# Kernel tuning notes

Measured on AMD Instinct MI355X. Metric: run time of the kernel, lower is better.

The kernel has to match this reference:

```python
import jax, jax.numpy as jnp
import numpy as np

N_NODES = 100000
N_EDGES = 1600000
D_IN = 128
D_OUT = 64
NUM_LAYERS = 3
BN_EPS = 1e-5


def setup_inputs() -> dict:
    key = jax.random.key(0)
    k_x, k_e, k_w = jax.random.split(key, 3)
    x = jax.random.normal(k_x, (N_NODES, D_IN), dtype=jnp.float32)
    edge_index = jax.random.randint(k_e, (2, N_EDGES), 0, N_NODES, dtype=jnp.int64)
    bn_gamma = jnp.ones((NUM_LAYERS, D_IN), dtype=jnp.float32)
    bn_beta = jnp.zeros((NUM_LAYERS, D_IN), dtype=jnp.float32)
    W = jax.random.normal(k_w, (D_IN, D_OUT), dtype=jnp.float32) * (1.0 / np.sqrt(D_IN))
    b = jnp.zeros((D_OUT,), dtype=jnp.float32)
    return {"x": x, "edge_index": edge_index, "bn_gamma": bn_gamma, "bn_beta": bn_beta, "W": W, "b": b}


def reference(x, edge_index, bn_gamma, bn_beta, W, b):
    # GNN forward, task='node', aggregate='sum', combine='sum', readout='sum',
    # recursive_weighting=False, training mode (no sigmoid, BN uses batch stats).
    n = x.shape[0]
    dst = edge_index[0]  # spmm(Adj, h): pooled[i] = sum over edges (i <- j) of h[j]
    src = edge_index[1]
    h = x
    for layer in range(NUM_LAYERS):
        # neighbor aggregate: sparse spmm == gather + segment-sum scatter
        agg = jax.ops.segment_sum(h[src], dst, num_segments=n)  # [N, D]
        # graph readout (single batched graph): sum over nodes, broadcast to every node
        readout = jnp.sum(h, axis=0, keepdims=True)  # [1, D]
        # functional 'sum' combine of (self, aggregated, readout)
        h = h + agg + readout
        # BatchNorm1d over the node dimension (training statistics, biased var)
        mean = jnp.mean(h, axis=0)
        var = jnp.var(h, axis=0)
        h = (h - mean) * jax.lax.rsqrt(var + BN_EPS) * bn_gamma[layer] + bn_beta[layer]
        h = jax.nn.relu(h)
    # node-task head (training branch: raw logits)
    return h @ W + b
```

## Files before the change

kernel.cpp:

```cpp
#include <hip/hip_runtime.h>

#define D 128
#define DOUT 64
#define BN_EPS 1e-5f
#define BCAP 96

#define NBK_SHIFT 8
#define NBK_MAX   512
#define SLOT_CAP  704
#define PA_E      4000

typedef unsigned int   u32;
typedef unsigned short u16;
typedef short  short8 __attribute__((ext_vector_type(8)));
typedef float  f32x4  __attribute__((ext_vector_type(4)));

__device__ __forceinline__ u16 f2bf(float f) {
    u32 x = __float_as_uint(f);
    x += 0x7fffu + ((x >> 16) & 1u);
    return (u16)(x >> 16);
}
__device__ __forceinline__ float bflo(u32 u) { return __uint_as_float(u << 16); }
__device__ __forceinline__ float bfhi(u32 u) { return __uint_as_float(u & 0xffff0000u); }

__global__ void init_kernel(const float* __restrict__ x, u16* __restrict__ xb,
                            int* __restrict__ bcnt,
                            float* __restrict__ sums,
                            const float* __restrict__ W, u16* __restrict__ wt,
                            int n_nodes, int n_ctr) {
    int total = n_nodes * (D / 4);
    for (int t = blockIdx.x * blockDim.x + threadIdx.x; t < total;
         t += gridDim.x * blockDim.x) {
        float4 v = ((const float4*)x)[t];
        ((ushort4*)xb)[t] = make_ushort4(f2bf(v.x), f2bf(v.y), f2bf(v.z), f2bf(v.w));
        if (t < n_ctr) bcnt[t] = 0;
        if (t < 3 * 8 * 256) sums[t] = 0.f;
        if (t < D * DOUT) {
            int c = t >> 7, k = t & (D - 1);
            wt[t] = f2bf(W[k * DOUT + c]);
        }
    }
}

__global__ __launch_bounds__(256) void partA_kernel(const int* __restrict__ ei,
                             int* __restrict__ bcnt,
                             u32* __restrict__ pairs, int n_edges, int n_bkt) {
    __shared__ u32 ord[PA_E];
    __shared__ u16 obkt[PA_E];
    __shared__ int hist[NBK_MAX];
    __shared__ int scanA[NBK_MAX], scanB[NBK_MAX];
    __shared__ int st[NBK_MAX], cur[NBK_MAX], gbase[NBK_MAX];

    const int tid  = threadIdx.x;
    const int slot = blockIdx.x & 7;
    const int e0   = blockIdx.x * PA_E;
    const int e1   = min(e0 + PA_E, n_edges);

    for (int i = tid; i < NBK_MAX; i += 256) hist[i] = 0;
    __syncthreads();
    for (int e = e0 + tid; e < e1; e += 256)
        atomicAdd(&hist[ei[e] >> NBK_SHIFT], 1);
    __syncthreads();
    for (int i = tid; i < NBK_MAX; i += 256) scanA[i] = hist[i];
    __syncthreads();
    int* a = scanA; int* b = scanB;
    for (int s = 1; s < NBK_MAX; s <<= 1) {
        for (int i = tid; i < NBK_MAX; i += 256)
            b[i] = a[i] + (i >= s ? a[i - s] : 0);
        __syncthreads();
        int* t_ = a; a = b; b = t_;
    }
    for (int x = tid; x < n_bkt; x += 256) {
        int c   = hist[x];
        int stx = a[x] - c;
        st[x] = stx; cur[x] = stx;
        gbase[x] = c ? atomicAdd(&bcnt[((x << 3) + slot) << 4], c) : 0;
    }
    __syncthreads();
    for (int e = e0 + tid; e < e1; e += 256) {
        int d = ei[e];
        int s = ei[n_edges + e];
        int x = d >> NBK_SHIFT;
        int pos = atomicAdd(&cur[x], 1);
        ord[pos]  = ((u32)(d & 255) << 17) | (u32)s;
        obkt[pos] = (u16)x;
    }
    __syncthreads();
    const int cntE = e1 - e0;
    for (int i = tid; i < cntE; i += 256) {
        int x   = obkt[i];
        int pos = gbase[x] + (i - st[x]);
        if (pos < SLOT_CAP)
            pairs[(size_t)((x << 3) + slot) * SLOT_CAP + pos] = ord[i];
    }
}

__global__ __launch_bounds__(256) void partB_kernel(const u32* __restrict__ pairs,
                             const int* __restrict__ bcnt,
                             int* __restrict__ deg, int* __restrict__ srcs,
                             int n_nodes) {
    __shared__ u32 lp[8 * SLOT_CAP];
    __shared__ int lsrc[8 * SLOT_CAP];
    __shared__ int cnt[256], st[256], cur[256];
    __shared__ int scanA[256], scanB[256];
    __shared__ int sofs[9];
    const int tid = threadIdx.x;
    int b = blockIdx.x;
    int node0 = b << NBK_SHIFT;
    if (tid == 0) {
        int acc = 0;
        for (int x = 0; x < 8; ++x) {
            sofs[x] = acc;
            acc += min(bcnt[((b << 3) + x) << 4], SLOT_CAP);
        }
        sofs[8] = acc;
    }
    cnt[tid] = 0;
    __syncthreads();
    for (int x = 0; x < 8; ++x) {
        int c0 = sofs[x], c1 = sofs[x + 1];
        const u32* src = pairs + (size_t)((b << 3) + x) * SLOT_CAP;
        for (int t = tid; t < c1 - c0; t += blockDim.x) {
            u32 pr = src[t];
            lp[c0 + t] = pr;
            atomicAdd(&cnt[pr >> 17], 1);
        }
    }
    __syncthreads();
    scanA[tid] = cnt[tid];
    __syncthreads();
    int* a = scanA; int* bb = scanB;
    for (int s = 1; s < 256; s <<= 1) {
        bb[tid] = a[tid] + (tid >= s ? a[tid - s] : 0);
        __syncthreads();
        int* t_ = a; a = bb; bb = t_;
    }
    st[tid] = a[tid] - cnt[tid];
    cur[tid] = st[tid];
    __syncthreads();
    int cntE = sofs[8];
    for (int t = tid; t < cntE; t += blockDim.x) {
        u32 pr = lp[t];
        int pos = atomicAdd(&cur[pr >> 17], 1);
        lsrc[pos] = (int)(pr & 0x1FFFFu);
    }
    __syncthreads();
    int grp = tid >> 4, lane = tid & 15;
    for (int li = grp; li < 256; li += 16) {
        int node = node0 + li;
        if (node < n_nodes) {
            int dg = cnt[li], s0 = st[li];
            for (int t = lane; t < dg; t += 16) {
                int key = lsrc[s0 + t];
                int rank = 0;
                for (int u = 0; u < dg; ++u) {
                    int o = lsrc[s0 + u];
                    rank += (o < key) || (o == key && u < t);
                }
                if (rank < BCAP) srcs[(size_t)node * BCAP + rank] = key;
            }
            if (lane == 0) deg[node] = dg;
        }
    }
}

template <bool APPLY>
__global__ void agg_kernel(const u16* __restrict__ h,
                           const int* __restrict__ srcs,
                           const int* __restrict__ deg,
                           const float* __restrict__ sums_prev,
                           const float* __restrict__ gam,
                           const float* __restrict__ bet,
                           float* __restrict__ sums_out,
                           u16* __restrict__ vout,
                           int n_nodes, float inv_n) {
    const int lane = threadIdx.x & 15;
    const int grp  = threadIdx.x >> 4;
    const int c    = lane << 3;
    float sc[8], sh[8];
    if (APPLY) {
        #pragma unroll
        for (int k = 0; k < 8; ++k) {
            int f = c + k;
            float S = 0.f, Q = 0.f;
            #pragma unroll
            for (int cp = 0; cp < 8; ++cp) {
                S += sums_prev[cp * 256 + f];
                Q += sums_prev[cp * 256 + 128 + f];
            }
            float mean = S * inv_n;
            float var  = fmaxf(Q * inv_n - mean * mean, 0.f);
            sc[k] = gam[f] * rsqrtf(var + BN_EPS);
            sh[k] = bet[f] - mean * sc[k];
        }
    }
    const int stride = gridDim.x * 16;
    float a[8];
    float s1[8] = {0,0,0,0,0,0,0,0};
    float s2[8] = {0,0,0,0,0,0,0,0};

#define ACC(u_) do { \
    float f0 = bflo((u_).x), f1 = bfhi((u_).x); \
    float f2 = bflo((u_).y), f3 = bfhi((u_).y); \
    float f4 = bflo((u_).z), f5 = bfhi((u_).z); \
    float f6 = bflo((u_).w), f7 = bfhi((u_).w); \
    if (APPLY) { \
        a[0] += fmaxf(fmaf(f0, sc[0], sh[0]), 0.f); \
        a[1] += fmaxf(fmaf(f1, sc[1], sh[1]), 0.f); \
        a[2] += fmaxf(fmaf(f2, sc[2], sh[2]), 0.f); \
        a[3] += fmaxf(fmaf(f3, sc[3], sh[3]), 0.f); \
        a[4] += fmaxf(fmaf(f4, sc[4], sh[4]), 0.f); \
        a[5] += fmaxf(fmaf(f5, sc[5], sh[5]), 0.f); \
        a[6] += fmaxf(fmaf(f6, sc[6], sh[6]), 0.f); \
        a[7] += fmaxf(fmaf(f7, sc[7], sh[7]), 0.f); \
    } else { \
        a[0] += f0; a[1] += f1; a[2] += f2; a[3] += f3; \
        a[4] += f4; a[5] += f5; a[6] += f6; a[7] += f7; \
    } } while (0)

    for (int i = blockIdx.x * 16 + grp; i < n_nodes; i += stride) {
        int off = i * BCAP;
        int dg  = min(deg[i], BCAP);
        {
            uint4 u = *(const uint4*)(h + ((size_t)i << 7) + c);
            float f0 = bflo(u.x), f1 = bfhi(u.x), f2 = bflo(u.y), f3 = bfhi(u.y);
            float f4 = bflo(u.z), f5 = bfhi(u.z), f6 = bflo(u.w), f7 = bfhi(u.w);
            float ff[8] = {f0, f1, f2, f3, f4, f5, f6, f7};
            #pragma unroll
            for (int k = 0; k < 8; ++k)
                a[k] = APPLY ? fmaxf(fmaf(ff[k], sc[k], sh[k]), 0.f) : ff[k];
        }
        for (int base = 0; base < dg; base += 16) {
            int cnt = min(dg - base, 16);
            int sv = (lane < cnt) ? srcs[off + base + lane] : 0;
            int svn = 0;
            int nb = base + 16;
            if (nb < dg && lane < min(dg - nb, 16)) svn = srcs[off + nb + lane];
            int k = 0;
            for (; k + 8 <= cnt; k += 8) {
                int j0 = __shfl(sv, k + 0, 16), j1 = __shfl(sv, k + 1, 16);
                int j2 = __shfl(sv, k + 2, 16), j3 = __shfl(sv, k + 3, 16);
                int j4 = __shfl(sv, k + 4, 16), j5 = __shfl(sv, k + 5, 16);
                int j6 = __shfl(sv, k + 6, 16), j7 = __shfl(sv, k + 7, 16);
                uint4 b0 = *(const uint4*)(h + ((size_t)j0 << 7) + c);
                uint4 b1 = *(const uint4*)(h + ((size_t)j1 << 7) + c);
                uint4 b2 = *(const uint4*)(h + ((size_t)j2 << 7) + c);
                uint4 b3 = *(const uint4*)(h + ((size_t)j3 << 7) + c);
                uint4 b4 = *(const uint4*)(h + ((size_t)j4 << 7) + c);
                uint4 b5 = *(const uint4*)(h + ((size_t)j5 << 7) + c);
                uint4 b6 = *(const uint4*)(h + ((size_t)j6 << 7) + c);
                uint4 b7 = *(const uint4*)(h + ((size_t)j7 << 7) + c);
                ACC(b0); ACC(b1); ACC(b2); ACC(b3);
                ACC(b4); ACC(b5); ACC(b6); ACC(b7);
            }
            for (; k + 4 <= cnt; k += 4) {
                int j0 = __shfl(sv, k + 0, 16), j1 = __shfl(sv, k + 1, 16);
                int j2 = __shfl(sv, k + 2, 16), j3 = __shfl(sv, k + 3, 16);
                uint4 b0 = *(const uint4*)(h + ((size_t)j0 << 7) + c);
                uint4 b1 = *(const uint4*)(h + ((size_t)j1 << 7) + c);
                uint4 b2 = *(const uint4*)(h + ((size_t)j2 << 7) + c);
                uint4 b3 = *(const uint4*)(h + ((size_t)j3 << 7) + c);
                ACC(b0); ACC(b1); ACC(b2); ACC(b3);
            }
            for (; k < cnt; ++k) {
                int j0 = __shfl(sv, k, 16);
                uint4 b0 = *(const uint4*)(h + ((size_t)j0 << 7) + c);
                ACC(b0);
            }
            sv = svn;
        }
        uint4 w;
        w.x = (u32)f2bf(a[0]) | ((u32)f2bf(a[1]) << 16);
        w.y = (u32)f2bf(a[2]) | ((u32)f2bf(a[3]) << 16);
        w.z = (u32)f2bf(a[4]) | ((u32)f2bf(a[5]) << 16);
        w.w = (u32)f2bf(a[6]) | ((u32)f2bf(a[7]) << 16);
        *(uint4*)(vout + ((size_t)i << 7) + c) = w;
        #pragma unroll
        for (int k = 0; k < 8; ++k) {
            s1[k] += a[k];
            s2[k] = fmaf(a[k], a[k], s2[k]);
        }
    }
#undef ACC

    __shared__ float redS[16][128];
    __shared__ float redQ[16][128];
    #pragma unroll
    for (int k = 0; k < 8; ++k) {
        redS[grp][c + k] = s1[k];
        redQ[grp][c + k] = s2[k];
    }
    __syncthreads();
    int tid = threadIdx.x;
    if (tid < 128) {
        float S = 0.f, Q = 0.f;
        #pragma unroll
        for (int g = 0; g < 16; ++g) { S += redS[g][tid]; Q += redQ[g][tid]; }
        int cp = blockIdx.x & 7;
        unsafeAtomicAdd(&sums_out[cp * 256 + tid], S);
        unsafeAtomicAdd(&sums_out[cp * 256 + 128 + tid], Q);
    }
}

__global__ __launch_bounds__(256) void head_mfma_kernel(
        const u16* __restrict__ v2, const float* __restrict__ sums2,
        const float* __restrict__ gam, const float* __restrict__ bet,
        const u16* __restrict__ wt, const float* __restrict__ b,
        float* __restrict__ out, int n_nodes, float inv_n) {
    const int wave = threadIdx.x >> 6;
    const int lane = threadIdx.x & 63;
    const int lo   = lane & 15;
    const int hi   = lane >> 4;

    short8 Bf[4][4];
    #pragma unroll
    for (int ct = 0; ct < 4; ++ct)
        #pragma unroll
        for (int ks = 0; ks < 4; ++ks)
            Bf[ct][ks] = *(const short8*)(wt + (ct * 16 + lo) * D + ks * 32 + hi * 8);

    float sc[4][8], sh[4][8];
    #pragma unroll
    for (int ks = 0; ks < 4; ++ks)
        #pragma unroll
        for (int j = 0; j < 8; ++j) {
            int f = ks * 32 + hi * 8 + j;
            float S = 0.f, Q = 0.f;
            #pragma unroll
            for (int cp = 0; cp < 8; ++cp) {
                S += sums2[cp * 256 + f];
                Q += sums2[cp * 256 + 128 + f];
            }
            float mean = S * inv_n;
            float var  = fmaxf(Q * inv_n - mean * mean, 0.f);
            sc[ks][j] = gam[f] * rsqrtf(var + BN_EPS);
            sh[ks][j] = bet[f] - mean * sc[ks][j];
        }
    float bias[4];
    #pragma unroll
    for (int ct = 0; ct < 4; ++ct) bias[ct] = b[ct * 16 + lo];

    const int nrt = (n_nodes + 15) >> 4;
    for (int rt = blockIdx.x * 4 + wave; rt < nrt; rt += gridDim.x * 4) {
        const int r0 = rt << 4;
        const int ar = min(r0 + lo, n_nodes - 1);
        const u16* hrow = v2 + ((size_t)ar << 7);
        f32x4 acc[4];
        #pragma unroll
        for (int ct = 0; ct < 4; ++ct) acc[ct] = (f32x4){0.f, 0.f, 0.f, 0.f};
        #pragma unroll
        for (int ks = 0; ks < 4; ++ks) {
            uint4 u = *(const uint4*)(hrow + ks * 32 + hi * 8);
            float f0 = bflo(u.x), f1 = bfhi(u.x), f2 = bflo(u.y), f3 = bfhi(u.y);
            float f4 = bflo(u.z), f5 = bfhi(u.z), f6 = bflo(u.w), f7 = bfhi(u.w);
            float w0 = fmaxf(fmaf(f0, sc[ks][0], sh[ks][0]), 0.f);
            float w1 = fmaxf(fmaf(f1, sc[ks][1], sh[ks][1]), 0.f);
            float w2 = fmaxf(fmaf(f2, sc[ks][2], sh[ks][2]), 0.f);
            float w3 = fmaxf(fmaf(f3, sc[ks][3], sh[ks][3]), 0.f);
            float w4 = fmaxf(fmaf(f4, sc[ks][4], sh[ks][4]), 0.f);
            float w5 = fmaxf(fmaf(f5, sc[ks][5], sh[ks][5]), 0.f);
            float w6 = fmaxf(fmaf(f6, sc[ks][6], sh[ks][6]), 0.f);
            float w7 = fmaxf(fmaf(f7, sc[ks][7], sh[ks][7]), 0.f);
            union { uint4 u4; short8 s8; } af;
            af.u4.x = (u32)f2bf(w0) | ((u32)f2bf(w1) << 16);
            af.u4.y = (u32)f2bf(w2) | ((u32)f2bf(w3) << 16);
            af.u4.z = (u32)f2bf(w4) | ((u32)f2bf(w5) << 16);
            af.u4.w = (u32)f2bf(w6) | ((u32)f2bf(w7) << 16);
            #pragma unroll
            for (int ct = 0; ct < 4; ++ct)
                acc[ct] = __builtin_amdgcn_mfma_f32_16x16x32_bf16(
                    af.s8, Bf[ct][ks], acc[ct], 0, 0, 0);
        }
        #pragma unroll
        for (int ct = 0; ct < 4; ++ct)
            #pragma unroll
            for (int rg = 0; rg < 4; ++rg) {
                int r = r0 + hi * 4 + rg;
                if (r < n_nodes)
                    out[(size_t)r * DOUT + ct * 16 + lo] = acc[ct][rg] + bias[ct];
            }
    }
}

extern "C" void kernel_launch(void* const* d_in, const int* in_sizes, int n_in,
                              void* d_out, int out_size, void* d_ws, size_t ws_size,
                              hipStream_t stream) {
    const float* x     = (const float*)d_in[0];
    const int*   ei    = (const int*)d_in[1];
    const float* gamma = (const float*)d_in[2];
    const float* beta  = (const float*)d_in[3];
    const float* W     = (const float*)d_in[4];
    const float* bvec  = (const float*)d_in[5];
    float* out = (float*)d_out;

    const int n_nodes = in_sizes[0] / D;
    const int n_edges = in_sizes[1] / 2;
    const int n_bkt   = (n_nodes + 255) >> 8;
    const int n_ctr   = n_bkt * 8 * 16;

    const size_t row_bytes = (size_t)n_nodes * D * sizeof(u16);
    char* p = (char*)d_ws;
    u16*   xb     = (u16*)p;   p += row_bytes;
    u16*   vA     = (u16*)p;   p += row_bytes;
    u16*   vB     = (u16*)p;   p += row_bytes;
    int*   srcs   = (int*)p;   p += (size_t)n_nodes * BCAP * sizeof(int);
    int*   deg    = (int*)p;   p += (size_t)n_nodes * sizeof(int);
    int*   bcnt   = (int*)p;   p += (size_t)n_ctr * sizeof(int);
    float* sums   = (float*)p;
    u16*   Wt     = (u16*)(p + 3 * 8 * 256 * sizeof(float));
    u32* pairs  = (u32*)vB;

    const float inv_n = 1.0f / (float)n_nodes;

    init_kernel<<<2048, 256, 0, stream>>>(x, xb, bcnt, sums, W, Wt, n_nodes, n_ctr);
    int pa_grid = ((n_edges + PA_E - 1) / PA_E + 7) & ~7;
    partA_kernel<<<pa_grid, 256, 0, stream>>>(ei, bcnt, pairs, n_edges, n_bkt);
    partB_kernel<<<n_bkt, 256, 0, stream>>>(pairs, bcnt, deg, srcs, n_nodes);

    const u16* h = xb;
    u16* vout = vA;
    for (int L = 0; L < 3; ++L) {
        float* sout = sums + (size_t)L * 2048;
        const float* sprev = (L > 0) ? sums + (size_t)(L - 1) * 2048 : nullptr;
        if (L == 0)
            agg_kernel<false><<<4096, 256, 0, stream>>>(h, srcs, deg,
                nullptr, nullptr, nullptr, sout, vout, n_nodes, inv_n);
        else
            agg_kernel<true><<<4096, 256, 0, stream>>>(h, srcs, deg,
                sprev, gamma + (size_t)(L - 1) * D, beta + (size_t)(L - 1) * D,
                sout, vout, n_nodes, inv_n);
        h = vout;
        vout = (vout == vA) ? vB : vA;
    }

    head_mfma_kernel<<<782, 256, 0, stream>>>(h, sums + 2 * 2048,
                                              gamma + 2 * D, beta + 2 * D,
                                              Wt, bvec, out, n_nodes, inv_n);
}
```

Measured before the change: 515.5 us.

## Split BatchNorm statistics out of aggregation kernel and drop 8-way gather unroll

The per-feature sum and sum-of-squares reduction, with its shared-memory buffers and atomics, moves out of agg_kernel into a separate stats_kernel that re-reads the bf16 output after each layer. The 8-wide gather unroll and the prefetch of the next index chunk are removed. The aim is to cut register and LDS pressure in the gather kernel so more waves can hide memory latency. In exchange it adds an extra read of the whole activation buffer plus one more launch per layer. The statistics are now computed from bf16-rounded values rather than fp32 accumulators.

Measured after the change: 460.7 us. -10.6%, faster.

```diff
diff --git a/kernel.cpp b/kernel.cpp
--- a/kernel.cpp
+++ b/kernel.cpp
@@ -171,7 +171,6 @@
                            const float* __restrict__ sums_prev,
                            const float* __restrict__ gam,
                            const float* __restrict__ bet,
-                           float* __restrict__ sums_out,
                            u16* __restrict__ vout,
                            int n_nodes, float inv_n) {
     const int lane = threadIdx.x & 15;
@@ -196,8 +195,6 @@
     }
     const int stride = gridDim.x * 16;
     float a[8];
-    float s1[8] = {0,0,0,0,0,0,0,0};
-    float s2[8] = {0,0,0,0,0,0,0,0};
 
 #define ACC(u_) do { \
     float f0 = bflo((u_).x), f1 = bfhi((u_).x); \
@@ -233,26 +230,7 @@
         for (int base = 0; base < dg; base += 16) {
             int cnt = min(dg - base, 16);
             int sv = (lane < cnt) ? srcs[off + base + lane] : 0;
-            int svn = 0;
-            int nb = base + 16;
-            if (nb < dg && lane < min(dg - nb, 16)) svn = srcs[off + nb + lane];
             int k = 0;
-            for (; k + 8 <= cnt; k += 8) {
-                int j0 = __shfl(sv, k + 0, 16), j1 = __shfl(sv, k + 1, 16);
-                int j2 = __shfl(sv, k + 2, 16), j3 = __shfl(sv, k + 3, 16);
-                int j4 = __shfl(sv, k + 4, 16), j5 = __shfl(sv, k + 5, 16);
-                int j6 = __shfl(sv, k + 6, 16), j7 = __shfl(sv, k + 7, 16);
-                uint4 b0 = *(const uint4*)(h + ((size_t)j0 << 7) + c);
-                uint4 b1 = *(const uint4*)(h + ((size_t)j1 << 7) + c);
-                uint4 b2 = *(const uint4*)(h + ((size_t)j2 << 7) + c);
-                uint4 b3 = *(const uint4*)(h + ((size_t)j3 << 7) + c);
-                uint4 b4 = *(const uint4*)(h + ((size_t)j4 << 7) + c);
-                uint4 b5 = *(const uint4*)(h + ((size_t)j5 << 7) + c);
-                uint4 b6 = *(const uint4*)(h + ((size_t)j6 << 7) + c);
-                uint4 b7 = *(const uint4*)(h + ((size_t)j7 << 7) + c);
-                ACC(b0); ACC(b1); ACC(b2); ACC(b3);
-                ACC(b4); ACC(b5); ACC(b6); ACC(b7);
-            }
             for (; k + 4 <= cnt; k += 4) {
                 int j0 = __shfl(sv, k + 0, 16), j1 = __shfl(sv, k + 1, 16);
                 int j2 = __shfl(sv, k + 2, 16), j3 = __shfl(sv, k + 3, 16);
@@ -267,7 +245,6 @@
                 uint4 b0 = *(const uint4*)(h + ((size_t)j0 << 7) + c);
                 ACC(b0);
             }
-            sv = svn;
         }
         uint4 w;
         w.x = (u32)f2bf(a[0]) | ((u32)f2bf(a[1]) << 16);
@@ -275,30 +252,38 @@
         w.z = (u32)f2bf(a[4]) | ((u32)f2bf(a[5]) << 16);
         w.w = (u32)f2bf(a[6]) | ((u32)f2bf(a[7]) << 16);
         *(uint4*)(vout + ((size_t)i << 7) + c) = w;
-        #pragma unroll
-        for (int k = 0; k < 8; ++k) {
-            s1[k] += a[k];
-            s2[k] = fmaf(a[k], a[k], s2[k]);
-        }
     }
 #undef ACC
-
-    __shared__ float redS[16][128];
-    __shared__ float redQ[16][128];
-    #pragma unroll
-    for (int k = 0; k < 8; ++k) {
-        redS[grp][c + k] = s1[k];
-        redQ[grp][c + k] = s2[k];
-    }
-    __syncthreads();
-    int tid = threadIdx.x;
-    if (tid < 128) {
-        float S = 0.f, Q = 0.f;
-        #pragma unroll
-        for (int g = 0; g < 16; ++g) { S += redS[g][tid]; Q += redQ[g][tid]; }
+}
+
+__global__ void stats_kernel(const u16* __restrict__ v,
+                             float* __restrict__ sums_cur, int n_nodes) {
+    int col = threadIdx.x & 63;
+    int sub = threadIdx.x >> 6;
+    float s1a = 0.f, s1b = 0.f, s2a = 0.f, s2b = 0.f;
+    const u32* vp = (const u32*)v;
+    for (int r = blockIdx.x * 4 + sub; r < n_nodes; r += gridDim.x * 4) {
+        u32 w = vp[(size_t)r * 64 + col];
+        float fa = bflo(w), fb = bfhi(w);
+        s1a += fa; s1b += fb; s2a += fa * fa; s2b += fb * fb;
+    }
+    __shared__ float red[4][64][4];
+    red[sub][col][0] = s1a; red[sub][col][1] = s1b;
+    red[sub][col][2] = s2a; red[sub][col][3] = s2b;
+    __syncthreads();
+    if (sub == 0) {
+        #pragma unroll
+        for (int m = 1; m < 4; ++m) {
+            red[0][col][0] += red[m][col][0];
+            red[0][col][1] += red[m][col][1];
+            red[0][col][2] += red[m][col][2];
+            red[0][col][3] += red[m][col][3];
+        }
         int cp = blockIdx.x & 7;
-        unsafeAtomicAdd(&sums_out[cp * 256 + tid], S);
-        unsafeAtomicAdd(&sums_out[cp * 256 + 128 + tid], Q);
+        unsafeAtomicAdd(&sums_cur[cp * 256 + 2 * col + 0], red[0][col][0]);
+        unsafeAtomicAdd(&sums_cur[cp * 256 + 2 * col + 1], red[0][col][1]);
+        unsafeAtomicAdd(&sums_cur[cp * 256 + 128 + 2 * col + 0], red[0][col][2]);
+        unsafeAtomicAdd(&sums_cur[cp * 256 + 128 + 2 * col + 1], red[0][col][3]);
     }
 }
 
@@ -424,11 +409,12 @@
         const float* sprev = (L > 0) ? sums + (size_t)(L - 1) * 2048 : nullptr;
         if (L == 0)
             agg_kernel<false><<<4096, 256, 0, stream>>>(h, srcs, deg,
-                nullptr, nullptr, nullptr, sout, vout, n_nodes, inv_n);
+                nullptr, nullptr, nullptr, vout, n_nodes, inv_n);
         else
             agg_kernel<true><<<4096, 256, 0, stream>>>(h, srcs, deg,
                 sprev, gamma + (size_t)(L - 1) * D, beta + (size_t)(L - 1) * D,
-                sout, vout, n_nodes, inv_n);
+                vout, n_nodes, inv_n);
+        stats_kernel<<<512, 256, 0, stream>>>(vout, sout, n_nodes);
         h = vout;
         vout = (vout == vA) ? vB : vA;
     }
```
